# Kernel tuning notes

Measured on AMD Instinct MI355X. Metric: run time of the kernel, lower is better.

## Reference

```python
import jax, jax.numpy as jnp
import numpy as np

EMBED_DIM = 1024
N_HEADS = 16
HEAD_DIM = EMBED_DIM // N_HEADS
B, S = 2, 2048


def setup_inputs() -> dict:
    key = jax.random.key(0)
    ks = jax.random.split(key, 8)
    scale = 1.0 / np.sqrt(EMBED_DIM)
    return {
        "key": jax.random.normal(ks[0], (B, S, EMBED_DIM), jnp.float32),
        "query": jax.random.normal(ks[1], (B, S, EMBED_DIM), jnp.float32),
        "value": jax.random.normal(ks[2], (B, S, EMBED_DIM), jnp.float32),
        # nn.Linear weights stored [out_features, in_features], applied as x @ W.T
        "Wq": jax.random.normal(ks[3], (EMBED_DIM, EMBED_DIM), jnp.float32) * scale,
        "Wk": jax.random.normal(ks[4], (EMBED_DIM, EMBED_DIM), jnp.float32) * scale,
        "Wv": jax.random.normal(ks[5], (EMBED_DIM, EMBED_DIM), jnp.float32) * scale,
        "Wo": jax.random.normal(ks[6], (EMBED_DIM, EMBED_DIM), jnp.float32) * scale,
        "bo": jax.random.normal(ks[7], (EMBED_DIM,), jnp.float32) * scale,
    }


def reference(key, query, value, Wq, Wk, Wv, Wo, bo) -> jnp.ndarray:
    b = key.shape[0]
    # project and split heads: [B, S, E] -> [B, H, S, D]
    def split_heads(x):
        return x.reshape(b, -1, N_HEADS, HEAD_DIM).transpose(0, 2, 1, 3)
    q = split_heads(query @ Wq.T)
    k = split_heads(key @ Wk.T)
    v = split_heads(value @ Wv.T)
    scores = jnp.einsum("bhqd,bhkd->bhqk", q, k) / np.sqrt(HEAD_DIM)
    attn = jax.nn.softmax(scores, axis=-1)
    ctx = jnp.einsum("bhqk,bhkd->bhqd", attn, v)  # [B, H, S, D]
    ctx = ctx.transpose(0, 2, 1, 3).reshape(b, -1, EMBED_DIM)
    return ctx @ Wo.T + bo
```

## Files before the change

kernel.cpp:

```cpp
#include <hip/hip_runtime.h>

typedef unsigned short u16;
typedef __bf16 bf8 __attribute__((ext_vector_type(8)));
typedef __bf16 bf2 __attribute__((ext_vector_type(2)));
typedef float f4 __attribute__((ext_vector_type(4)));

typedef __attribute__((address_space(1))) const unsigned int gas_u32;
typedef __attribute__((address_space(3))) unsigned int las_u32;
#define ASYNC16(g, l) __builtin_amdgcn_global_load_lds((gas_u32*)(g), (las_u32*)(l), 16, 0, 0)

__device__ __forceinline__ unsigned pkbf(float lo, float hi) {
    union { bf2 v; unsigned u; } t;
    t.v[0] = (__bf16)lo;
    t.v[1] = (__bf16)hi;
    return t.u;
}

__device__ __forceinline__ u16 bf1(float f) {
    union { __bf16 v; u16 u; } t;
    t.v = (__bf16)f;
    return t.u;
}

__device__ __forceinline__ float fexp2(float x) {
#if __has_builtin(__builtin_amdgcn_exp2f)
  return __builtin_amdgcn_exp2f(x);
#else
  return __expf(x * 0.69314718056f);
#endif
}

__global__ __launch_bounds__(256) void cvt_all(
    const float* __restrict__ k_, const float* __restrict__ q_, const float* __restrict__ v_,
    const float* __restrict__ wq, const float* __restrict__ wk, const float* __restrict__ wv,
    const float* __restrict__ wo, u16* __restrict__ ws) {
  size_t e = ((size_t)blockIdx.x * 256 + threadIdx.x) * 8;
  const float* src;
  if      (e <  4194304) src = k_ + e;
  else if (e <  8388608) src = q_ + (e - 4194304);
  else if (e < 12582912) src = v_ + (e - 8388608);
  else if (e < 13631488) src = wq + (e - 12582912);
  else if (e < 14680064) src = wk + (e - 13631488);
  else if (e < 15728640) src = wv + (e - 14680064);
  else                   src = wo + (e - 15728640);
  float4 f0 = ((const float4*)src)[0];
  float4 f1 = ((const float4*)src)[1];
  uint4 o;
  o.x = pkbf(f0.x, f0.y);
  o.y = pkbf(f0.z, f0.w);
  o.z = pkbf(f1.x, f1.y);
  o.w = pkbf(f1.z, f1.w);
  *(uint4*)(ws + e) = o;
}

template<int BM, bool FINAL>
__device__ __forceinline__ void gemm_tile(const u16* __restrict__ A, const u16* __restrict__ Bm,
                                          u16* __restrict__ Cb, float* __restrict__ Cf,
                                          const float* __restrict__ bias, float scale,
                                          int bm, int bn, int ldc) {
  __shared__ u16 As[BM*64];
  __shared__ u16 Bs[128*64];
  const int tid = threadIdx.x;
  const int wave = tid >> 6, lane = tid & 63;
  const int wm = wave >> 1, wn = wave & 1;
  const int quad = lane >> 4, l16 = lane & 15;
  const int MI = BM / 32;

  f4 acc[MI][4];
  const f4 zz = {0.f, 0.f, 0.f, 0.f};
  #pragma unroll
  for (int i = 0; i < MI; i++)
    #pragma unroll
    for (int j = 0; j < 4; j++) acc[i][j] = zz;

  const int kr = tid >> 3;
  const int cs = (tid & 7) ^ (kr & 7);
  const u16* ga = A  + (size_t)(bm*BM  + kr)*1024 + cs*8;
  const u16* gb = Bm + (size_t)(bn*128 + kr)*1024 + cs*8;
  u16* la = As + tid*8;
  u16* lb = Bs + tid*8;

  for (int kt = 0; kt < 1024; kt += 64) {
    #pragma unroll
    for (int p = 0; p < BM/32; p++) ASYNC16(ga + (size_t)(p*32)*1024 + kt, la + p*2048);
    #pragma unroll
    for (int p = 0; p < 4; p++)     ASYNC16(gb + (size_t)(p*32)*1024 + kt, lb + p*2048);
    __syncthreads();
    #pragma unroll
    for (int kk = 0; kk < 2; kk++) {
      bf8 af[MI];
      #pragma unroll
      for (int mi = 0; mi < MI; mi++)
        af[mi] = *(const bf8*)(As + (wm*(BM/2) + mi*16 + l16)*64 + (((kk*4 + quad) ^ (l16 & 7))*8));
      #pragma unroll
      for (int ni = 0; ni < 4; ni++) {
        bf8 bfr = *(const bf8*)(Bs + (wn*64 + ni*16 + l16)*64 + (((kk*4 + quad) ^ (l16 & 7))*8));
        #pragma unroll
        for (int mi = 0; mi < MI; mi++)
          acc[mi][ni] = __builtin_amdgcn_mfma_f32_16x16x32_bf16(af[mi], bfr, acc[mi][ni], 0, 0, 0);
      }
    }
    __syncthreads();
  }

  #pragma unroll
  for (int mi = 0; mi < MI; mi++)
    #pragma unroll
    for (int ni = 0; ni < 4; ni++) {
      const int col = bn*128 + wn*64 + ni*16 + l16;
      #pragma unroll
      for (int r = 0; r < 4; r++) {
        const int row = bm*BM + wm*(BM/2) + mi*16 + quad*4 + r;
        if (FINAL) Cf[(size_t)row*ldc + col] = acc[mi][ni][r] + bias[col];
        else       Cb[(size_t)row*ldc + col] = bf1(acc[mi][ni][r] * scale);
      }
    }
}

#define QSCALE 0.180336880f

__global__ __launch_bounds__(256, 3) void gemm_qkv(
    const u16* __restrict__ xq, const u16* __restrict__ xk, const u16* __restrict__ xv,
    const u16* __restrict__ wq, const u16* __restrict__ wk, const u16* __restrict__ wv,
    u16* __restrict__ Qo, u16* __restrict__ Ko, u16* __restrict__ Vto) {
  if (blockIdx.z == 0)
    gemm_tile<128,false>(xq, wq, Qo, nullptr, nullptr, QSCALE, blockIdx.x, blockIdx.y, 1024);
  else if (blockIdx.z == 1)
    gemm_tile<128,false>(xk, wk, Ko, nullptr, nullptr, 1.0f, blockIdx.x, blockIdx.y, 1024);
  else
    gemm_tile<128,false>(wv, xv, Vto, nullptr, nullptr, 1.0f, blockIdx.y, blockIdx.x, 4096);
}

__global__ __launch_bounds__(256, 2) void gemm_out(
    const u16* __restrict__ ctx, const u16* __restrict__ wo,
    const float* __restrict__ bias, float* __restrict__ out) {
  gemm_tile<64,true>(ctx, wo, nullptr, out, bias, 1.0f, blockIdx.x, blockIdx.y, 1024);
}

#define KSW(r) (((((r) >> 3) & 1) << 2) | ((r) & 3))
__global__ __launch_bounds__(256, 4) void flash_attn(
    const u16* __restrict__ Qg, const u16* __restrict__ Kg,
    const u16* __restrict__ Vtg, u16* __restrict__ ctx) {
  __shared__ uint4 smem4[2208];
  u16* Ks = (u16*)smem4;
  u16* Vt = (u16*)smem4 + 8192;
  float* Of = (float*)smem4;
  float* Lf = (float*)smem4 + 2*64*68;

  const int tid = threadIdx.x;
  const int wave = tid >> 6, lane = tid & 63;
  const int quad = lane >> 4, l16 = lane & 15;
  const int wq = wave >> 1, wk = wave & 1;
  const int h = blockIdx.x, qt = blockIdx.y, b = blockIdx.z;

  bf8 qf[2][2];
  {
    const u16* qp = Qg + (size_t)(b*2048 + qt*64 + wq*32)*1024 + h*64;
    #pragma unroll
    for (int qs = 0; qs < 2; qs++)
      #pragma unroll
      for (int kc = 0; kc < 2; kc++)
        qf[qs][kc] = *(const bf8*)(qp + (size_t)(qs*16 + l16)*1024 + kc*32 + quad*8);
  }

  const f4 zz = {0.f, 0.f, 0.f, 0.f};
  f4 ot[4][2];
  float lrow[2] = {0.f, 0.f};
  #pragma unroll
  for (int ds = 0; ds < 4; ds++)
    #pragma unroll
    for (int qs = 0; qs < 2; qs++) ot[ds][qs] = zz;

  const int kr = tid >> 3;
  const u16* kga = Kg + (size_t)(b*2048 + kr)*1024 + h*64 + ((tid & 7) ^ KSW(kr))*8;
  const int vd = tid >> 4;
  const u16* vga = Vtg + (size_t)(h*64 + vd)*4096 + b*2048 + (((tid & 15) ^ vd))*8;
  u16* kld = Ks + tid*8;
  u16* vld = Vt + tid*8;

  const int prow0 = ((l16 >> 2) << 3) + (l16 & 3);
  const int prow1 = prow0 + 4;
  const int ksw   = (((l16 >> 2) & 1) << 2) | (l16 & 3);

  for (int kv0 = 0; kv0 < 2048; kv0 += 128) {
    __syncthreads();
    #pragma unroll
    for (int p = 0; p < 4; p++) ASYNC16(kga + (size_t)(kv0 + p*32)*1024, kld + p*2048);
    #pragma unroll
    for (int p = 0; p < 4; p++) ASYNC16(vga + (size_t)(p*16)*4096 + kv0, vld + p*2048);
    __syncthreads();

    #pragma unroll
    for (int kb = 0; kb < 2; kb++) {
      f4 st[2][2];
      #pragma unroll
      for (int f = 0; f < 2; f++)
        #pragma unroll
        for (int qs = 0; qs < 2; qs++) st[f][qs] = zz;
      __builtin_amdgcn_s_setprio(1);
      #pragma unroll
      for (int f = 0; f < 2; f++) {
        const int row = wk*64 + kb*32 + (f ? prow1 : prow0);
        #pragma unroll
        for (int kc = 0; kc < 2; kc++) {
          bf8 kf = *(const bf8*)(Ks + row*64 + (((kc*4 + quad) ^ ksw)*8));
          #pragma unroll
          for (int qs = 0; qs < 2; qs++)
            st[f][qs] = __builtin_amdgcn_mfma_f32_16x16x32_bf16(kf, qf[qs][kc], st[f][qs], 0, 0, 0);
        }
      }
      __builtin_amdgcn_s_setprio(0);
      bf8 pf[2];
      #pragma unroll
      for (int qs = 0; qs < 2; qs++) {
        float p0 = fexp2(st[0][qs][0]), p1 = fexp2(st[0][qs][1]);
        float p2 = fexp2(st[0][qs][2]), p3 = fexp2(st[0][qs][3]);
        float p4 = fexp2(st[1][qs][0]), p5 = fexp2(st[1][qs][1]);
        float p6 = fexp2(st[1][qs][2]), p7 = fexp2(st[1][qs][3]);
        lrow[qs] += ((p0 + p1) + (p2 + p3)) + ((p4 + p5) + (p6 + p7));
        union { uint4 u; bf8 v; } pu;
        pu.u.x = pkbf(p0, p1);
        pu.u.y = pkbf(p2, p3);
        pu.u.z = pkbf(p4, p5);
        pu.u.w = pkbf(p6, p7);
        pf[qs] = pu.v;
      }
      __builtin_amdgcn_s_setprio(1);
      #pragma unroll
      for (int ds = 0; ds < 4; ds++) {
        const int d = ds*16 + l16;
        bf8 vf = *(const bf8*)(Vt + d*128 + (((wk*8 + kb*4 + quad) ^ l16)*8));
        #pragma unroll
        for (int qs = 0; qs < 2; qs++)
          ot[ds][qs] = __builtin_amdgcn_mfma_f32_16x16x32_bf16(vf, pf[qs], ot[ds][qs], 0, 0, 0);
      }
      __builtin_amdgcn_s_setprio(0);
    }
  }

  __syncthreads();
  #pragma unroll
  for (int qs = 0; qs < 2; qs++) {
    lrow[qs] += __shfl_xor(lrow[qs], 16);
    lrow[qs] += __shfl_xor(lrow[qs], 32);
  }
  float* Ofw = Of + wk*(64*68);
  #pragma unroll
  for (int ds = 0; ds < 4; ds++)
    #pragma unroll
    for (int qs = 0; qs < 2; qs++)
      #pragma unroll
      for (int r = 0; r < 4; r++)
        Ofw[(wq*32 + qs*16 + l16)*68 + ds*16 + quad*4 + r] = ot[ds][qs][r];
  if (quad == 0) {
    Lf[wk*64 + wq*32 + l16]      = lrow[0];
    Lf[wk*64 + wq*32 + 16 + l16] = lrow[1];
  }
  __syncthreads();
  {
    const int qr = tid >> 2, dp = (tid & 3)*16;
    const float inv = 1.f / (Lf[qr] + Lf[64 + qr]);
    const float* o0 = Of + qr*68 + dp;
    const float* o1 = o0 + 64*68;
    unsigned ow[8];
    #pragma unroll
    for (int i = 0; i < 8; i++)
      ow[i] = pkbf((o0[2*i] + o1[2*i]) * inv, (o0[2*i+1] + o1[2*i+1]) * inv);
    u16* cp = ctx + (size_t)(b*2048 + qt*64 + qr)*1024 + h*64 + dp;
    *(uint4*)cp       = *(uint4*)&ow[0];
    *(uint4*)(cp + 8) = *(uint4*)&ow[4];
  }
}

extern "C" void kernel_launch(void* const* d_in, const int* in_sizes, int n_in,
                              void* d_out, int out_size, void* d_ws, size_t ws_size,
                              hipStream_t stream) {
  const float* key_  = (const float*)d_in[0];
  const float* query = (const float*)d_in[1];
  const float* value = (const float*)d_in[2];
  const float* Wq = (const float*)d_in[3];
  const float* Wk = (const float*)d_in[4];
  const float* Wv = (const float*)d_in[5];
  const float* Wo = (const float*)d_in[6];
  const float* bo = (const float*)d_in[7];
  float* out = (float*)d_out;

  u16* ws  = (u16*)d_ws;
  u16* xkb = ws;
  u16* xqb = ws + 4194304;
  u16* xvb = ws + 8388608;
  u16* Wqb = ws + 12582912;
  u16* Wkb = ws + 13631488;
  u16* Wvb = ws + 14680064;
  u16* Wob = ws + 15728640;
  u16* Qb  = ws + 16777216;
  u16* Kb  = ws + 20971520;
  u16* Vtb = ws + 25165824;
  u16* Cb  = ws + 29360128;

  cvt_all<<<8192, 256, 0, stream>>>(key_, query, value, Wq, Wk, Wv, Wo, ws);
  gemm_qkv<<<dim3(32, 8, 3), 256, 0, stream>>>(xqb, xkb, xvb, Wqb, Wkb, Wvb, Qb, Kb, Vtb);
  flash_attn<<<dim3(16, 32, 2), 256, 0, stream>>>(Qb, Kb, Vtb, Cb);
  gemm_out<<<dim3(64, 8), 256, 0, stream>>>(Cb, Wob, bo, out);
}
```

Before: 200.9 us.

## Double-buffer K/V tiles in flash attention with async prefetch

New measurement: 199.0 us. No clear change (-0.9%).

```diff
diff --git a/kernel.cpp b/kernel.cpp
--- a/kernel.cpp
+++ b/kernel.cpp
@@ -142,8 +142,7 @@
     const u16* __restrict__ Qg, const u16* __restrict__ Kg,
     const u16* __restrict__ Vtg, u16* __restrict__ ctx) {
   __shared__ uint4 smem4[2208];
-  u16* Ks = (u16*)smem4;
-  u16* Vt = (u16*)smem4 + 8192;
+  u16* S = (u16*)smem4;
   float* Of = (float*)smem4;
   float* Lf = (float*)smem4 + 2*64*68;
 
@@ -173,69 +172,81 @@
 
   const int kr = tid >> 3;
   const u16* kga = Kg + (size_t)(b*2048 + kr)*1024 + h*64 + ((tid & 7) ^ KSW(kr))*8;
-  const int vd = tid >> 4;
-  const u16* vga = Vtg + (size_t)(h*64 + vd)*4096 + b*2048 + (((tid & 15) ^ vd))*8;
-  u16* kld = Ks + tid*8;
-  u16* vld = Vt + tid*8;
+  const int vd = tid >> 3;
+  const u16* vga = Vtg + (size_t)(h*64 + vd)*4096 + b*2048 + ((tid & 7) ^ (vd & 7))*8;
 
   const int prow0 = ((l16 >> 2) << 3) + (l16 & 3);
   const int prow1 = prow0 + 4;
   const int ksw   = (((l16 >> 2) & 1) << 2) | (l16 & 3);
 
-  for (int kv0 = 0; kv0 < 2048; kv0 += 128) {
-    __syncthreads();
-    #pragma unroll
-    for (int p = 0; p < 4; p++) ASYNC16(kga + (size_t)(kv0 + p*32)*1024, kld + p*2048);
-    #pragma unroll
-    for (int p = 0; p < 4; p++) ASYNC16(vga + (size_t)(p*16)*4096 + kv0, vld + p*2048);
-    __syncthreads();
-
-    #pragma unroll
-    for (int kb = 0; kb < 2; kb++) {
-      f4 st[2][2];
-      #pragma unroll
-      for (int f = 0; f < 2; f++)
-        #pragma unroll
-        for (int qs = 0; qs < 2; qs++) st[f][qs] = zz;
-      __builtin_amdgcn_s_setprio(1);
-      #pragma unroll
-      for (int f = 0; f < 2; f++) {
-        const int row = wk*64 + kb*32 + (f ? prow1 : prow0);
-        #pragma unroll
-        for (int kc = 0; kc < 2; kc++) {
-          bf8 kf = *(const bf8*)(Ks + row*64 + (((kc*4 + quad) ^ ksw)*8));
-          #pragma unroll
-          for (int qs = 0; qs < 2; qs++)
-            st[f][qs] = __builtin_amdgcn_mfma_f32_16x16x32_bf16(kf, qf[qs][kc], st[f][qs], 0, 0, 0);
-        }
-      }
-      __builtin_amdgcn_s_setprio(0);
-      bf8 pf[2];
-      #pragma unroll
-      for (int qs = 0; qs < 2; qs++) {
-        float p0 = fexp2(st[0][qs][0]), p1 = fexp2(st[0][qs][1]);
-        float p2 = fexp2(st[0][qs][2]), p3 = fexp2(st[0][qs][3]);
-        float p4 = fexp2(st[1][qs][0]), p5 = fexp2(st[1][qs][1]);
-        float p6 = fexp2(st[1][qs][2]), p7 = fexp2(st[1][qs][3]);
-        lrow[qs] += ((p0 + p1) + (p2 + p3)) + ((p4 + p5) + (p6 + p7));
-        union { uint4 u; bf8 v; } pu;
-        pu.u.x = pkbf(p0, p1);
-        pu.u.y = pkbf(p2, p3);
-        pu.u.z = pkbf(p4, p5);
-        pu.u.w = pkbf(p6, p7);
-        pf[qs] = pu.v;
-      }
-      __builtin_amdgcn_s_setprio(1);
-      #pragma unroll
-      for (int ds = 0; ds < 4; ds++) {
-        const int d = ds*16 + l16;
-        bf8 vf = *(const bf8*)(Vt + d*128 + (((wk*8 + kb*4 + quad) ^ l16)*8));
+  #pragma unroll
+  for (int p = 0; p < 2; p++) ASYNC16(kga + (size_t)(p*32)*1024, S + tid*8 + p*2048);
+  #pragma unroll
+  for (int p = 0; p < 2; p++) ASYNC16(vga + (size_t)(p*32)*4096, S + 4096 + tid*8 + p*2048);
+
+  for (int t = 0; t < 32; t++) {
+    const u16* Ks = S + (t & 1)*8192;
+    const u16* Vt = Ks + 4096;
+    if (t < 31) {
+      u16* kd = S + ((t + 1) & 1)*8192 + tid*8;
+      const int kv1 = (t + 1)*64;
+      #pragma unroll
+      for (int p = 0; p < 2; p++) ASYNC16(kga + (size_t)(kv1 + p*32)*1024, kd + p*2048);
+      #pragma unroll
+      for (int p = 0; p < 2; p++) ASYNC16(vga + (size_t)(p*32)*4096 + kv1, kd + 4096 + p*2048);
+      asm volatile("s_waitcnt vmcnt(4)" ::: "memory");
+    } else {
+      asm volatile("s_waitcnt vmcnt(0)" ::: "memory");
+    }
+    __builtin_amdgcn_sched_barrier(0);
+    __builtin_amdgcn_s_barrier();
+
+    f4 st[2][2];
+    #pragma unroll
+    for (int f = 0; f < 2; f++)
+      #pragma unroll
+      for (int qs = 0; qs < 2; qs++) st[f][qs] = zz;
+    __builtin_amdgcn_s_setprio(1);
+    #pragma unroll
+    for (int f = 0; f < 2; f++) {
+      const int row = wk*32 + (f ? prow1 : prow0);
+      #pragma unroll
+      for (int kc = 0; kc < 2; kc++) {
+        bf8 kf = *(const bf8*)(Ks + row*64 + (((kc*4 + quad) ^ ksw)*8));
         #pragma unroll
         for (int qs = 0; qs < 2; qs++)
-          ot[ds][qs] = __builtin_amdgcn_mfma_f32_16x16x32_bf16(vf, pf[qs], ot[ds][qs], 0, 0, 0);
+          st[f][qs] = __builtin_amdgcn_mfma_f32_16x16x32_bf16(kf, qf[qs][kc], st[f][qs], 0, 0, 0);
       }
-      __builtin_amdgcn_s_setprio(0);
-    }
+    }
+    __builtin_amdgcn_s_setprio(0);
+    bf8 pf[2];
+    #pragma unroll
+    for (int qs = 0; qs < 2; qs++) {
+      float p0 = fexp2(st[0][qs][0]), p1 = fexp2(st[0][qs][1]);
+      float p2 = fexp2(st[0][qs][2]), p3 = fexp2(st[0][qs][3]);
+      float p4 = fexp2(st[1][qs][0]), p5 = fexp2(st[1][qs][1]);
+      float p6 = fexp2(st[1][qs][2]), p7 = fexp2(st[1][qs][3]);
+      lrow[qs] += ((p0 + p1) + (p2 + p3)) + ((p4 + p5) + (p6 + p7));
+      union { uint4 u; bf8 v; } pu;
+      pu.u.x = pkbf(p0, p1);
+      pu.u.y = pkbf(p2, p3);
+      pu.u.z = pkbf(p4, p5);
+      pu.u.w = pkbf(p6, p7);
+      pf[qs] = pu.v;
+    }
+    __builtin_amdgcn_s_setprio(1);
+    #pragma unroll
+    for (int ds = 0; ds < 4; ds++) {
+      const int d = ds*16 + l16;
+      bf8 vf = *(const bf8*)(Vt + d*64 + (((wk*4 + quad) ^ (l16 & 7))*8));
+      #pragma unroll
+      for (int qs = 0; qs < 2; qs++)
+        ot[ds][qs] = __builtin_amdgcn_mfma_f32_16x16x32_bf16(vf, pf[qs], ot[ds][qs], 0, 0, 0);
+    }
+    __builtin_amdgcn_s_setprio(0);
+
+    asm volatile("s_waitcnt lgkmcnt(0)" ::: "memory");
+    __builtin_amdgcn_s_barrier();
   }
 
   __syncthreads();
```
